# Optimization experiments

Measured on AMD Instinct MI355X. Metric: run time of the kernel, lower is better.

Reference implementation:

```python
import jax, jax.numpy as jnp
import numpy as np

DIM = 4096
N_HEADS = 32
N_KV_HEADS = 8
HEAD_DIM = DIM // N_HEADS      # 128
N_REP = N_HEADS // N_KV_HEADS  # 4
B, S = 2, 2048
THETA = 10000.0


def _rope_tables(seq_len, head_dim):
    # standard llama2.c freqs: [1, S, 1, head_dim//2]
    freqs = 1.0 / (THETA ** (np.arange(0, head_dim, 2, dtype=np.float32) / head_dim))
    t = np.arange(seq_len, dtype=np.float32)
    ang = np.outer(t, freqs)  # [S, head_dim//2]
    cos = jnp.asarray(np.cos(ang))[None, :, None, :]
    sin = jnp.asarray(np.sin(ang))[None, :, None, :]
    return cos, sin


def setup_inputs() -> dict:
    key = jax.random.key(0)
    ks = jax.random.split(key, 5)
    x = jax.random.normal(ks[0], (B, S, DIM), dtype=jnp.float32)
    freqs_cos, freqs_sin = _rope_tables(S, HEAD_DIM)
    scale = 1.0 / np.sqrt(DIM)
    wq = jax.random.normal(ks[1], (DIM, N_HEADS * HEAD_DIM), dtype=jnp.float32) * scale
    wk = jax.random.normal(ks[2], (DIM, N_KV_HEADS * HEAD_DIM), dtype=jnp.float32) * scale
    wv = jax.random.normal(ks[3], (DIM, N_KV_HEADS * HEAD_DIM), dtype=jnp.float32) * scale
    wo = jax.random.normal(ks[4], (N_HEADS * HEAD_DIM, DIM), dtype=jnp.float32) * scale
    return {"x": x, "freqs_cos": freqs_cos, "freqs_sin": freqs_sin,
            "wq": wq, "wk": wk, "wv": wv, "wo": wo}


def _apply_rotary(t, cos, sin):
    # t: [B, S, H, head_dim]; cos/sin: [1, S, 1, head_dim//2]
    b, s, h, d = t.shape
    tr = t.reshape(b, s, h, d // 2, 2)
    t_r, t_i = tr[..., 0], tr[..., 1]
    out_r = t_r * cos - t_i * sin
    out_i = t_r * sin + t_i * cos
    return jnp.stack([out_r, out_i], axis=-1).reshape(b, s, h, d)


def reference(x, freqs_cos, freqs_sin, wq, wk, wv, wo):
    b, s, _ = x.shape
    q = (x @ wq).reshape(b, s, N_HEADS, HEAD_DIM)
    k = (x @ wk).reshape(b, s, N_KV_HEADS, HEAD_DIM)
    v = (x @ wv).reshape(b, s, N_KV_HEADS, HEAD_DIM)
    q = _apply_rotary(q, freqs_cos, freqs_sin)
    k = _apply_rotary(k, freqs_cos, freqs_sin)
    # GQA: repeat kv heads to match q heads
    k = jnp.repeat(k, N_REP, axis=2)  # [b, s, H, hd]
    v = jnp.repeat(v, N_REP, axis=2)
    # NOTE: source calls SDPA with attn_mask=None and no is_causal -> non-causal
    scores = jnp.einsum('bqhd,bkhd->bhqk', q, k) / jnp.sqrt(
        jnp.asarray(HEAD_DIM, dtype=q.dtype))
    attn = jax.nn.softmax(scores, axis=-1)
    out = jnp.einsum('bhqk,bkhd->bqhd', attn, v)
    out = out.reshape(b, s, N_HEADS * HEAD_DIM)
    return out @ wo
```

## Files before the change

### kernel.cpp

```cpp
#include <hip/hip_runtime.h>
#include <cstdint>


typedef __attribute__((ext_vector_type(8))) short short8;
typedef __attribute__((ext_vector_type(4))) float f32x4;
typedef __attribute__((ext_vector_type(16))) float f32x16;

__device__ __forceinline__ float bf2f(unsigned short u) {
  union { unsigned int i; float f; } v; v.i = ((unsigned int)u) << 16; return v.f;
}
__device__ __forceinline__ unsigned short f2bf(float f) {
  union { float f; unsigned int i; } v; v.f = f;
  unsigned int r = v.i + 0x7fffu + ((v.i >> 16) & 1u);
  return (unsigned short)(r >> 16);
}

__device__ __forceinline__ void gload_lds16(const void* g, void* lds) {
  __builtin_amdgcn_global_load_lds(
      (const __attribute__((address_space(1))) unsigned int*)g,
      (__attribute__((address_space(3))) unsigned int*)lds, 16, 0, 0);
}

__device__ __forceinline__ unsigned int cvtpk_bf16(float lo, float hi) {
  unsigned int r;
  asm("v_cvt_pk_bf16_f32 %0, %1, %2" : "=v"(r) : "v"(lo), "v"(hi));
  return r;
}
__device__ __forceinline__ void pl32swap(unsigned int& a, unsigned int& b) {
  asm("v_permlane32_swap_b32 %0, %1" : "+v"(a), "+v"(b));
}


__global__ __launch_bounds__(256) void prepass(const float* __restrict__ x,
                                               const float* __restrict__ wq,
                                               const float* __restrict__ wk,
                                               const float* __restrict__ wv,
                                               const float* __restrict__ wo,
                                               unsigned short* __restrict__ xbf,
                                               unsigned short* __restrict__ wqkvT,
                                               unsigned short* __restrict__ woT) {
  __shared__ float tile[32][33];
  const int b = blockIdx.x;
  if (b < 16384) {
    size_t i = (size_t)b * 256 + threadIdx.x;
    float4 v = ((const float4*)x)[i];
    ushort4 o; o.x = f2bf(v.x); o.y = f2bf(v.y); o.z = f2bf(v.z); o.w = f2bf(v.w);
    ((ushort4*)xbf)[i] = o;
    return;
  }
  int tx = threadIdx.x & 31, ty = threadIdx.x >> 5;
  const float* src; int c0, C, gc0, r0;
  unsigned short* dst; int ldd;
  if (b < 16384 + 24576) {
    int t = b - 16384;
    gc0 = (t % 192) * 32; r0 = (t / 192) * 32;
    if (gc0 < 4096)      { src = wq; c0 = gc0;        C = 4096; }
    else if (gc0 < 5120) { src = wk; c0 = gc0 - 4096; C = 1024; }
    else                 { src = wv; c0 = gc0 - 5120; C = 1024; }
    dst = wqkvT; ldd = 4096;
  } else {
    int t = b - 40960;
    gc0 = (t % 128) * 32; r0 = (t / 128) * 32;
    src = wo; c0 = gc0; C = 4096;
    dst = woT; ldd = 4096;
  }
#pragma unroll
  for (int j = 0; j < 4; ++j)
    tile[ty + j * 8][tx] = src[(size_t)(r0 + ty + j * 8) * C + c0 + tx];
  __syncthreads();
#pragma unroll
  for (int j = 0; j < 4; ++j)
    dst[(size_t)(gc0 + ty + j * 8) * ldd + r0 + tx] = f2bf(tile[tx][ty + j * 8]);
}

__global__ __launch_bounds__(256) void rope_kk(unsigned short* __restrict__ qkv,
                                               const float* __restrict__ cosT,
                                               const float* __restrict__ sinT) {
  int idx = blockIdx.x * 256 + threadIdx.x;
  int t = idx >> 7;
  int cb = (idx & 127) * 8;
  int s = t & 2047;
  int j0 = (cb & 127) >> 1;
  unsigned short* p = qkv + (size_t)t * 6144 + 4096 + cb;
  uint4 u = *(const uint4*)p;
  float4 c4 = *(const float4*)&cosT[s * 64 + j0];
  float4 s4 = *(const float4*)&sinT[s * 64 + j0];
  auto rot = [](unsigned int& uu, float c, float sn) {
    float re = bf2f((unsigned short)(uu & 0xffffu));
    float im = bf2f((unsigned short)(uu >> 16));
    float nr = re * c - im * sn;
    float ni = re * sn + im * c;
    uu = (unsigned int)f2bf(nr) | ((unsigned int)f2bf(ni) << 16);
  };
  rot(u.x, c4.x, s4.x); rot(u.y, c4.y, s4.y);
  rot(u.z, c4.z, s4.z); rot(u.w, c4.w, s4.w);
  *(uint4*)p = u;
}


#define GBAR() asm volatile("s_barrier" ::: "memory")
#define GVM6() asm volatile("s_waitcnt vmcnt(6)" ::: "memory")
#define GVM4() asm volatile("s_waitcnt vmcnt(4)" ::: "memory")
#define GHINT() asm volatile("s_waitcnt lgkmcnt(8)" ::: "memory")

#define GLDA(buf, mh)                                                                   \
  do {                                                                                  \
    _Pragma("unroll") for (int m_ = 0; m_ < 4; ++m_)                                    \
    _Pragma("unroll") for (int ks_ = 0; ks_ < 2; ++ks_)                                 \
      a[m_][ks_] = *(const short8*)&smem[buf][0]                                        \
          [(wm * 128 + (mh) * 64 + m_ * 16 + lr) * 64 + (((ks_ * 4 + lg) ^ (lr & 7)) << 3)]; \
  } while (0)

#define GLDB(bf_, buf, nh)                                                              \
  do {                                                                                  \
    _Pragma("unroll") for (int n_ = 0; n_ < 2; ++n_)                                    \
    _Pragma("unroll") for (int ks_ = 0; ks_ < 2; ++ks_)                                 \
      bf_[n_][ks_] = *(const short8*)&smem[buf][1]                                      \
          [(wn * 64 + (nh) * 32 + n_ * 16 + lr) * 64 + (((ks_ * 4 + lg) ^ (lr & 7)) << 3)]; \
  } while (0)

#define GMM(bf_, mh, nh)                                                                \
  do {                                                                                  \
    __builtin_amdgcn_s_setprio(1);                                                      \
    _Pragma("unroll") for (int ks_ = 0; ks_ < 2; ++ks_)                                 \
    _Pragma("unroll") for (int m_ = 0; m_ < 4; ++m_)                                    \
    _Pragma("unroll") for (int n_ = 0; n_ < 2; ++n_)                                    \
      acc[(mh) * 4 + m_][(nh) * 2 + n_] = __builtin_amdgcn_mfma_f32_16x16x32_bf16(      \
          a[m_][ks_], bf_[n_][ks_], acc[(mh) * 4 + m_][(nh) * 2 + n_], 0, 0, 0);        \
    __builtin_amdgcn_s_setprio(0);                                                      \
  } while (0)

#define GSTG(half, buf, tile)                                                           \
  do {                                                                                  \
    _Pragma("unroll") for (int t2_ = 0; t2_ < 2; ++t2_)                                 \
      gload_lds16(srcp[half][t2_] + ((size_t)(tile) << 6),                              \
                  &smem[buf][(half) >> 1][dsto[half][t2_]]);                            \
  } while (0)

template <typename OutT>
__device__ __forceinline__ void gemm256_body(const unsigned short* __restrict__ A,
                                             const unsigned short* __restrict__ B,
                                             OutT* __restrict__ C, int K, int ldc,
                                             int bid,
                                             unsigned short (*smem)[2][16384]) {
  const int xcd = bid & 7, ii = bid >> 3;
  const int mt = (xcd & 3) * 4 + (ii & 3);
  const int nt = (xcd >> 2) * 8 + (ii >> 2);
  const int m0 = mt * 256, n0 = nt * 256;
  const int tid = threadIdx.x, w = tid >> 6, l = tid & 63;
  const int wm = w >> 2, wn = w & 3;
  const int lr = l & 15, lg = l >> 4;
  const int NT = K >> 6;

  const int lsub = l >> 3, lgr = l & 7;
  const int sg = (lgr ^ lsub) << 3;
  const unsigned short* srcp[4][2];
  int dsto[4][2];
#pragma unroll
  for (int t2 = 0; t2 < 2; ++t2) {
    int lb = t2 * 64 + w * 8;
    int pa0 = (lb & 63) + ((lb >> 6) << 7);
    int pb0 = (lb & 31) + ((lb >> 5) << 6);
    srcp[0][t2] = A + (size_t)(m0 + pa0 + lsub) * K + sg;       dsto[0][t2] = pa0 * 64;
    srcp[1][t2] = A + (size_t)(m0 + pa0 + 64 + lsub) * K + sg;  dsto[1][t2] = (pa0 + 64) * 64;
    srcp[2][t2] = B + (size_t)(n0 + pb0 + lsub) * K + sg;       dsto[2][t2] = pb0 * 64;
    srcp[3][t2] = B + (size_t)(n0 + pb0 + 32 + lsub) * K + sg;  dsto[3][t2] = (pb0 + 32) * 64;
  }

  f32x4 acc[8][4] = {};
  short8 a[4][2], b0f[2][2], b1f[2][2];

  GSTG(0, 0, 0); GSTG(2, 0, 0); GSTG(3, 0, 0); GSTG(1, 0, 0);
  GSTG(0, 1, 1); GSTG(2, 1, 1); GSTG(3, 1, 1);
  GVM6();
  GBAR();

  for (int t = 0; t < NT / 2; ++t) {
    const int t1 = 2 * t + 1;
    const int t2a = (2 * t + 2 < NT) ? 2 * t + 2 : NT - 1;
    const int t2b = (2 * t + 3 < NT) ? 2 * t + 3 : NT - 1;
    GLDA(0, 0); GLDB(b0f, 0, 0);
    GSTG(1, 1, t1);
    GHINT();
    GBAR(); GMM(b0f, 0, 0); GBAR();
    GLDB(b1f, 0, 1);
    GSTG(0, 0, t2a);
    GBAR(); GMM(b1f, 0, 1); GBAR();
    GLDA(0, 1);
    GSTG(2, 0, t2a);
    GBAR(); GMM(b0f, 1, 0); GBAR();
    GSTG(3, 0, t2a);
    GBAR(); GMM(b1f, 1, 1); GVM6(); GBAR();
    GLDA(1, 0); GLDB(b0f, 1, 0);
    GSTG(1, 0, t2a);
    GHINT();
    GBAR(); GMM(b0f, 0, 0); GBAR();
    GLDB(b1f, 1, 1);
    GSTG(0, 1, t2b);
    GBAR(); GMM(b1f, 0, 1); GBAR();
    GLDA(1, 1);
    GSTG(2, 1, t2b);
    GBAR(); GMM(b0f, 1, 0); GBAR();
    GSTG(3, 1, t2b);
    GBAR(); GMM(b1f, 1, 1); GVM6(); GBAR();
  }

#pragma unroll
  for (int m = 0; m < 8; ++m)
#pragma unroll
    for (int n = 0; n < 4; ++n)
#pragma unroll
      for (int r = 0; r < 4; ++r) {
        int row = m0 + wm * 128 + m * 16 + lg * 4 + r;
        int col = n0 + wn * 64 + n * 16 + lr;
        float v = acc[m][n][r];
        if constexpr (sizeof(OutT) == 2)
          C[(size_t)row * ldc + col] = (OutT)f2bf(v);
        else
          C[(size_t)row * ldc + col] = v;
      }
}


#define KLDA(buf)                                                                       \
  do {                                                                                  \
    _Pragma("unroll") for (int m_ = 0; m_ < 4; ++m_)                                    \
    _Pragma("unroll") for (int ks_ = 0; ks_ < 2; ++ks_)                                 \
      a2[m_][ks_] = *(const short8*)&As2[buf]                                           \
          [(wm * 64 + m_ * 16 + lr) * 64 + (((ks_ * 4 + lg) ^ (lr & 7)) << 3)];         \
  } while (0)

#define KLDB(bf_, buf, nh)                                                              \
  do {                                                                                  \
    _Pragma("unroll") for (int n_ = 0; n_ < 2; ++n_)                                    \
    _Pragma("unroll") for (int ks_ = 0; ks_ < 2; ++ks_)                                 \
      bf_[n_][ks_] = *(const short8*)&Bs2[buf]                                          \
          [(wn * 64 + (nh) * 32 + n_ * 16 + lr) * 64 + (((ks_ * 4 + lg) ^ (lr & 7)) << 3)]; \
  } while (0)

#define KMM(bf_, nh)                                                                    \
  do {                                                                                  \
    __builtin_amdgcn_s_setprio(1);                                                      \
    _Pragma("unroll") for (int ks_ = 0; ks_ < 2; ++ks_)                                 \
    _Pragma("unroll") for (int m_ = 0; m_ < 4; ++m_)                                    \
    _Pragma("unroll") for (int n_ = 0; n_ < 2; ++n_)                                    \
      acc[m_][(nh) * 2 + n_] = __builtin_amdgcn_mfma_f32_16x16x32_bf16(                 \
          a2[m_][ks_], bf_[n_][ks_], acc[m_][(nh) * 2 + n_], 0, 0, 0);                  \
    __builtin_amdgcn_s_setprio(0);                                                      \
  } while (0)

#define KSTGA(buf, tile)                                                                \
  do {                                                                                  \
    _Pragma("unroll") for (int t2_ = 0; t2_ < 2; ++t2_)                                 \
      gload_lds16(srcA[t2_] + ((size_t)(tile) << 6), &As2[buf][dstA[t2_]]);             \
  } while (0)
#define KSTGB0(buf, tile)                                                               \
  do {                                                                                  \
    _Pragma("unroll") for (int t2_ = 0; t2_ < 2; ++t2_)                                 \
      gload_lds16(srcB0[t2_] + ((size_t)(tile) << 6), &Bs2[buf][dstB0[t2_]]);           \
  } while (0)
#define KSTGB1(buf, tile)                                                               \
  do {                                                                                  \
    _Pragma("unroll") for (int t2_ = 0; t2_ < 2; ++t2_)                                 \
      gload_lds16(srcB1[t2_] + ((size_t)(tile) << 6), &Bs2[buf][dstB1[t2_]]);           \
  } while (0)

__device__ __forceinline__ void kvproj_body(const unsigned short* __restrict__ A,
                                            const unsigned short* __restrict__ B,
                                            unsigned short* __restrict__ C,
                                            unsigned short* __restrict__ vt,
                                            int K, int ldc, int bid,
                                            unsigned short (*As2)[8192],
                                            unsigned short (*Bs2)[16384]) {
  const int xcd = bid & 7, ii = bid >> 3;
  const int mt = (xcd & 3) * 8 + (ii & 7);
  const int nt = (xcd >> 2) * 4 + (ii >> 3);
  const int m0 = mt * 128, n0 = nt * 256;
  const int tid = threadIdx.x, w = tid >> 6, l = tid & 63;
  const int wm = w >> 2, wn = w & 3;
  const int lr = l & 15, lg = l >> 4;
  const int NT = K >> 6;

  const int lsub = l >> 3, lgr = l & 7;
  const int sg = (lgr ^ lsub) << 3;
  const unsigned short* srcA[2];  int dstA[2];
  const unsigned short* srcB0[2]; int dstB0[2];
  const unsigned short* srcB1[2]; int dstB1[2];
#pragma unroll
  for (int t2 = 0; t2 < 2; ++t2) {
    int ra = t2 * 64 + w * 8;
    srcA[t2] = A + (size_t)(m0 + ra + lsub) * K + sg;            dstA[t2] = ra * 64;
    int lb = t2 * 64 + w * 8;
    int pb0 = (lb & 31) + ((lb >> 5) << 6);
    srcB0[t2] = B + (size_t)(n0 + pb0 + lsub) * K + sg;          dstB0[t2] = pb0 * 64;
    srcB1[t2] = B + (size_t)(n0 + pb0 + 32 + lsub) * K + sg;     dstB1[t2] = (pb0 + 32) * 64;
  }

  f32x4 acc[4][4] = {};
  short8 a2[4][2], bb0[2][2], bb1[2][2];

  KSTGA(0, 0); KSTGB0(0, 0); KSTGB1(0, 0);
  KSTGA(1, 1); KSTGB0(1, 1);
  GVM4();
  GBAR();

  for (int t = 0; t < NT / 2; ++t) {
    const int t1 = 2 * t + 1;
    const int t2a = (2 * t + 2 < NT) ? 2 * t + 2 : NT - 1;
    const int t2b = (2 * t + 3 < NT) ? 2 * t + 3 : NT - 1;
    KLDA(0); KLDB(bb0, 0, 0);
    KSTGB1(1, t1);
    GHINT();
    GBAR(); KMM(bb0, 0); GBAR();
    KLDB(bb1, 0, 1);
    KSTGA(0, t2a); KSTGB0(0, t2a);
    GBAR(); KMM(bb1, 1); GVM4(); GBAR();
    KLDA(1); KLDB(bb0, 1, 0);
    KSTGB1(0, t2a);
    GHINT();
    GBAR(); KMM(bb0, 0); GBAR();
    KLDB(bb1, 1, 1);
    KSTGA(1, t2b); KSTGB0(1, t2b);
    GBAR(); KMM(bb1, 1); GVM4(); GBAR();
  }

  if (n0 >= 1024) {
#pragma unroll
    for (int m = 0; m < 4; ++m)
#pragma unroll
      for (int n = 0; n < 4; ++n) {
        const int col = n0 + wn * 64 + n * 16 + lr;
        const int kvh = (col - 1024) >> 7, d = (col - 1024) & 127;
        const int row0 = m0 + wm * 64 + m * 16 + lg * 4;
        const int bb = row0 >> 11, tok = row0 & 2047;
        ushort4 o;
        o.x = f2bf(acc[m][n][0]); o.y = f2bf(acc[m][n][1]);
        o.z = f2bf(acc[m][n][2]); o.w = f2bf(acc[m][n][3]);
        *(ushort4*)&vt[(size_t)((bb * 8 + kvh) * 128 + d) * 2048 + tok] = o;
      }
  } else {
#pragma unroll
    for (int m = 0; m < 4; ++m)
#pragma unroll
      for (int n = 0; n < 4; ++n)
#pragma unroll
        for (int r = 0; r < 4; ++r) {
          int row = m0 + wm * 64 + m * 16 + lg * 4 + r;
          int col = n0 + wn * 64 + n * 16 + lr;
          C[(size_t)row * ldc + col] = f2bf(acc[m][n][r]);
        }
  }
}

__global__ __launch_bounds__(512) void gemm_qkv(const unsigned short* __restrict__ A,
                                                const unsigned short* __restrict__ Bq,
                                                const unsigned short* __restrict__ Bkv,
                                                unsigned short* __restrict__ qkv,
                                                unsigned short* __restrict__ vt) {
  __shared__ unsigned short smem[2][2][16384];
  const int bid = blockIdx.x;
  if (bid < 256) {
    gemm256_body<unsigned short>(A, Bq, qkv, 4096, 6144, bid, smem);
  } else {
    unsigned short (*As2)[8192]  = (unsigned short (*)[8192])&smem[0][0][0];
    unsigned short (*Bs2)[16384] = (unsigned short (*)[16384])(&smem[0][0][0] + 16384);
    kvproj_body(A, Bkv, qkv + 4096, vt, 4096, 6144, bid - 256, As2, Bs2);
  }
}

__global__ __launch_bounds__(512) void gemm_oproj(const unsigned short* __restrict__ A,
                                                  const unsigned short* __restrict__ B,
                                                  float* __restrict__ C,
                                                  int K, int ldc) {
  __shared__ unsigned short smem[2][2][16384];
  gemm256_body<float>(A, B, C, K, ldc, blockIdx.x, smem);
}


__global__ __launch_bounds__(256, 2) void attn_k(const unsigned short* __restrict__ qkv,
                                                 const unsigned short* __restrict__ vt,
                                                 const float* __restrict__ fc,
                                                 const float* __restrict__ fs,
                                                 unsigned short* __restrict__ ctx) {
  __shared__ unsigned short Ks[2][64 * 128];
  __shared__ unsigned short Vs[3][128 * 64];
  const int bid = blockIdx.x;
  const int xcd = bid & 7, idx = bid >> 3;
  const int kvg = xcd * 2 + (idx >> 6);
  const int hg = (idx >> 4) & 3;
  const int qt = idx & 15;
  const int b = kvg >> 3, kvh = kvg & 7, h = kvh * 4 + hg;
  const int w = threadIdx.x >> 6, l = threadIdx.x & 63;
  const int lc = l & 31, hi = l >> 5;
  const size_t tok0 = (size_t)b * 2048;
  const int q0 = qt * 128 + w * 32;
  const float C2 = 0.12751744516557944f;

  const unsigned short* ksrc[4];
  const unsigned short* vsrc[4];
#pragma unroll
  for (int i = 0; i < 4; ++i) {
    int L = w * 256 + i * 64 + l;
    int krow = L >> 4, kc = L & 15;
    ksrc[i] = qkv + (tok0 + krow) * 6144 + 4096 + kvh * 128 + ((kc ^ (krow & 7)) << 3);
    int vrow = L >> 3, vc = L & 7;
    vsrc[i] = vt + (size_t)(kvg * 128 + vrow) * 2048 + ((vc ^ (vrow & 7)) << 3);
  }
  const int ldsBase = (w * 256) * 8;

  auto stageK = [&](int bufi, int kv0s) {
#pragma unroll
    for (int i = 0; i < 4; ++i)
      gload_lds16(ksrc[i] + (size_t)kv0s * 6144, &Ks[bufi][ldsBase + i * 512]);
  };
  auto stageV = [&](int bufi, int kv0s) {
#pragma unroll
    for (int i = 0; i < 4; ++i)
      gload_lds16(vsrc[i] + kv0s, &Vs[bufi][ldsBase + i * 512]);
  };

  const unsigned short* Qb = qkv + (tok0 + q0 + lc) * 6144 + h * 128 + hi * 8;
  const int s = q0 + lc;
  short8 qf[8];
#pragma unroll
  for (int dc = 0; dc < 8; ++dc) {
    uint4 raw = *(const uint4*)(Qb + dc * 16);
    float4 c4 = *(const float4*)&fc[s * 64 + dc * 8 + hi * 4];
    float4 s4 = *(const float4*)&fs[s * 64 + dc * 8 + hi * 4];
    auto rotw = [C2](unsigned int uu, float c, float sn) -> unsigned int {
      float re = bf2f((unsigned short)(uu & 0xffffu));
      float im = bf2f((unsigned short)(uu >> 16));
      return cvtpk_bf16((re * c - im * sn) * C2, (re * sn + im * c) * C2);
    };
    union { unsigned int u[4]; short8 v; } t;
    t.u[0] = rotw(raw.x, c4.x, s4.x);
    t.u[1] = rotw(raw.y, c4.y, s4.y);
    t.u[2] = rotw(raw.z, c4.z, s4.z);
    t.u[3] = rotw(raw.w, c4.w, s4.w);
    qf[dc] = t.v;
  }

  f32x16 acc[4] = {};
  float lsum = 0.f;

  stageK(0, 0);
  stageV(0, 0);
  stageV(1, 64);
  __syncthreads();

  int kb = 0, vb = 0;
  const int swz = (lc & 7) << 3;
  for (int kt = 0; kt < 32; ++kt) {
    const int nk = (kt + 1 < 32) ? kt + 1 : 31;
    const int nv = (kt + 2 < 32) ? kt + 2 : 31;
    int vs2 = vb + 2; if (vs2 >= 3) vs2 -= 3;
    stageK(kb ^ 1, nk * 64);
    stageV(vs2, nv * 64);
    f32x16 s0 = {}, s1 = {};
    __builtin_amdgcn_s_setprio(1);
#pragma unroll
    for (int dc = 0; dc < 8; ++dc) {
      int cidx = ((dc * 2 + hi) << 3) ^ swz;
      short8 kf0 = *(const short8*)&Ks[kb][lc * 128 + cidx];
      short8 kf1 = *(const short8*)&Ks[kb][(lc + 32) * 128 + cidx];
      s0 = __builtin_amdgcn_mfma_f32_32x32x16_bf16(kf0, qf[dc], s0, 0, 0, 0);
      s1 = __builtin_amdgcn_mfma_f32_32x32x16_bf16(kf1, qf[dc], s1, 0, 0, 0);
    }
    __builtin_amdgcn_s_setprio(0);
    float p[32];
    short8 pa[4];
#pragma unroll
    for (int g = 0; g < 4; ++g) {
#pragma unroll
      for (int j = 0; j < 8; ++j) {
        float sv = (g < 2) ? s0[g * 8 + j] : s1[(g - 2) * 8 + j];
        p[g * 8 + j] = __builtin_amdgcn_exp2f(sv);
      }
      unsigned int c0 = cvtpk_bf16(p[g * 8 + 0], p[g * 8 + 1]);
      unsigned int c1 = cvtpk_bf16(p[g * 8 + 2], p[g * 8 + 3]);
      unsigned int c2 = cvtpk_bf16(p[g * 8 + 4], p[g * 8 + 5]);
      unsigned int c3 = cvtpk_bf16(p[g * 8 + 6], p[g * 8 + 7]);
      pl32swap(c0, c2);
      pl32swap(c1, c3);
      union { unsigned int u[4]; short8 v; } t;
      t.u[0] = c0; t.u[1] = c1; t.u[2] = c2; t.u[3] = c3;
      pa[g] = t.v;
    }
    __builtin_amdgcn_s_setprio(1);
#pragma unroll
    for (int ks = 0; ks < 4; ++ks) {
#pragma unroll
      for (int dt = 0; dt < 4; ++dt) {
        short8 vf = *(const short8*)&Vs[vb][(dt * 32 + lc) * 64 + ((((ks * 2 + hi) << 3) ^ swz))];
        acc[dt] = __builtin_amdgcn_mfma_f32_32x32x16_bf16(pa[ks], vf, acc[dt], 0, 0, 0);
      }
    }
    __builtin_amdgcn_s_setprio(0);
#pragma unroll
    for (int r = 0; r < 32; ++r) lsum += p[r];
    asm volatile("s_waitcnt vmcnt(4)" ::: "memory");
    asm volatile("s_barrier" ::: "memory");
    kb ^= 1;
    vb = (vb + 1 == 3) ? 0 : vb + 1;
  }
  lsum += __shfl_xor(lsum, 32, 64);
  float rl = 1.0f / lsum;
#pragma unroll
  for (int r = 0; r < 16; ++r) {
    int crow = (r & 3) + 8 * (r >> 2) + 4 * hi;
    float rlr = __shfl(rl, crow, 64);
    unsigned short* cp = ctx + (tok0 + q0 + crow) * 4096 + h * 128 + lc;
#pragma unroll
    for (int dt = 0; dt < 4; ++dt) cp[dt * 32] = f2bf(acc[dt][r] * rlr);
  }
}


extern "C" void kernel_launch(void* const* d_in, const int* in_sizes, int n_in,
                              void* d_out, int out_size, void* d_ws, size_t ws_size,
                              hipStream_t stream) {
  const float* x  = (const float*)d_in[0];
  const float* fc = (const float*)d_in[1];
  const float* fs = (const float*)d_in[2];
  const float* wq = (const float*)d_in[3];
  const float* wk = (const float*)d_in[4];
  const float* wv = (const float*)d_in[5];
  const float* wo = (const float*)d_in[6];
  float* out = (float*)d_out;
  char* ws = (char*)d_ws;

  constexpr size_t SZ_WQKVT = (size_t)6144 * 4096 * 2;
  constexpr size_t SZ_WOT   = (size_t)4096 * 4096 * 2;
  constexpr size_t SZ_QKV   = (size_t)4096 * 6144 * 2;
  constexpr size_t SZ_VT    = (size_t)16 * 128 * 2048 * 2;

  unsigned short* wqkvT = (unsigned short*)ws;
  unsigned short* woT   = (unsigned short*)(ws + SZ_WQKVT);
  unsigned short* qkv   = (unsigned short*)(ws + SZ_WQKVT + SZ_WOT);
  unsigned short* vt    = (unsigned short*)(ws + SZ_WQKVT + SZ_WOT + SZ_QKV);
  unsigned short* xbf   = (unsigned short*)(ws + SZ_WQKVT + SZ_WOT + SZ_QKV + SZ_VT);
  unsigned short* ctx   = xbf;

  prepass<<<57344, 256, 0, stream>>>(x, wq, wk, wv, wo, xbf, wqkvT, woT);
  gemm_qkv<<<512, 512, 0, stream>>>(xbf, wqkvT, wqkvT + (size_t)4096 * 4096, qkv, vt);
  rope_kk<<<2048, 256, 0, stream>>>(qkv, fc, fs);
  attn_k<<<1024, 256, 0, stream>>>(qkv, vt, fc, fs, ctx);
  gemm_oproj<<<256, 512, 0, stream>>>(ctx, woT, out, 4096, 4096);
}
```

Baseline: 496.4 us.

## Split-K the KV projection into uniform 256x256 tiles with a reduce kernel

The KV projection blocks in the QKV GEMM launch now reuse the 256x256 gemm body with split-K=2, so all 512 blocks run the same tile shape and get balanced work. The two bf16 partial sums are written to a workspace, and a new reduce kernel adds them, applies RoPE to K and transposes V into the vt layout. This replaces the separate kvproj path and rope kernel when the workspace is large enough. In exchange it adds extra global traffic for the partials, an extra rounding of the partials to bf16, and a transpose kernel.

Measured after the change: 496.4 us. No clear change (+0.0%).

```diff
diff --git a/kernel.cpp b/kernel.cpp
--- a/kernel.cpp
+++ b/kernel.cpp
@@ -97,6 +97,57 @@
   *(uint4*)p = u;
 }
 
+__global__ __launch_bounds__(256) void reduce_kv(const unsigned short* __restrict__ p0,
+                                                 const unsigned short* __restrict__ p1,
+                                                 unsigned short* __restrict__ qkv,
+                                                 unsigned short* __restrict__ vt,
+                                                 const float* __restrict__ cosT,
+                                                 const float* __restrict__ sinT) {
+  __shared__ float tile[32][33];
+  const int b = blockIdx.x;
+  if (b < 2048) {
+    int idx = b * 256 + threadIdx.x;
+    int t = idx >> 7;
+    int cb = (idx & 127) * 8;
+    int s = t & 2047;
+    int j0 = (cb & 127) >> 1;
+    const size_t off = (size_t)t * 2048 + cb;
+    uint4 u0 = *(const uint4*)(p0 + off);
+    uint4 u1 = *(const uint4*)(p1 + off);
+    float4 c4 = *(const float4*)&cosT[s * 64 + j0];
+    float4 s4 = *(const float4*)&sinT[s * 64 + j0];
+    auto comb = [](unsigned int a, unsigned int bb, float c, float sn) -> unsigned int {
+      float re = bf2f((unsigned short)(a & 0xffffu)) + bf2f((unsigned short)(bb & 0xffffu));
+      float im = bf2f((unsigned short)(a >> 16)) + bf2f((unsigned short)(bb >> 16));
+      float nr = re * c - im * sn;
+      float ni = re * sn + im * c;
+      return (unsigned int)f2bf(nr) | ((unsigned int)f2bf(ni) << 16);
+    };
+    uint4 o;
+    o.x = comb(u0.x, u1.x, c4.x, s4.x);
+    o.y = comb(u0.y, u1.y, c4.y, s4.y);
+    o.z = comb(u0.z, u1.z, c4.z, s4.z);
+    o.w = comb(u0.w, u1.w, c4.w, s4.w);
+    *(uint4*)(qkv + (size_t)t * 6144 + 4096 + cb) = o;
+    return;
+  }
+  const int t = b - 2048;
+  const int tok0t = (t & 63) * 32;
+  const int d0 = ((t >> 6) & 3) * 32;
+  const int bk = t >> 8;
+  const int bb = bk >> 3, kvh = bk & 7;
+  const int tx = threadIdx.x & 31, ty = threadIdx.x >> 5;
+#pragma unroll
+  for (int j = 0; j < 4; ++j) {
+    size_t off = (size_t)(bb * 2048 + tok0t + ty + j * 8) * 2048 + 1024 + kvh * 128 + d0 + tx;
+    tile[ty + j * 8][tx] = bf2f(p0[off]) + bf2f(p1[off]);
+  }
+  __syncthreads();
+#pragma unroll
+  for (int j = 0; j < 4; ++j)
+    vt[(size_t)(bk * 128 + d0 + ty + j * 8) * 2048 + tok0t + tx] = f2bf(tile[tx][ty + j * 8]);
+}
+
 
 #define GBAR() asm volatile("s_barrier" ::: "memory")
 #define GVM6() asm volatile("s_waitcnt vmcnt(6)" ::: "memory")
@@ -140,17 +191,13 @@
 template <typename OutT>
 __device__ __forceinline__ void gemm256_body(const unsigned short* __restrict__ A,
                                              const unsigned short* __restrict__ B,
-                                             OutT* __restrict__ C, int K, int ldc,
-                                             int bid,
+                                             OutT* __restrict__ C, int Kext, int lda,
+                                             int ldc, int m0, int n0,
                                              unsigned short (*smem)[2][16384]) {
-  const int xcd = bid & 7, ii = bid >> 3;
-  const int mt = (xcd & 3) * 4 + (ii & 3);
-  const int nt = (xcd >> 2) * 8 + (ii >> 2);
-  const int m0 = mt * 256, n0 = nt * 256;
   const int tid = threadIdx.x, w = tid >> 6, l = tid & 63;
   const int wm = w >> 2, wn = w & 3;
   const int lr = l & 15, lg = l >> 4;
-  const int NT = K >> 6;
+  const int NT = Kext >> 6;
 
   const int lsub = l >> 3, lgr = l & 7;
   const int sg = (lgr ^ lsub) << 3;
@@ -161,10 +208,10 @@
     int lb = t2 * 64 + w * 8;
     int pa0 = (lb & 63) + ((lb >> 6) << 7);
     int pb0 = (lb & 31) + ((lb >> 5) << 6);
-    srcp[0][t2] = A + (size_t)(m0 + pa0 + lsub) * K + sg;       dsto[0][t2] = pa0 * 64;
-    srcp[1][t2] = A + (size_t)(m0 + pa0 + 64 + lsub) * K + sg;  dsto[1][t2] = (pa0 + 64) * 64;
-    srcp[2][t2] = B + (size_t)(n0 + pb0 + lsub) * K + sg;       dsto[2][t2] = pb0 * 64;
-    srcp[3][t2] = B + (size_t)(n0 + pb0 + 32 + lsub) * K + sg;  dsto[3][t2] = (pb0 + 32) * 64;
+    srcp[0][t2] = A + (size_t)(m0 + pa0 + lsub) * lda + sg;       dsto[0][t2] = pa0 * 64;
+    srcp[1][t2] = A + (size_t)(m0 + pa0 + 64 + lsub) * lda + sg;  dsto[1][t2] = (pa0 + 64) * 64;
+    srcp[2][t2] = B + (size_t)(n0 + pb0 + lsub) * lda + sg;       dsto[2][t2] = pb0 * 64;
+    srcp[3][t2] = B + (size_t)(n0 + pb0 + 32 + lsub) * lda + sg;  dsto[3][t2] = (pb0 + 32) * 64;
   }
 
   f32x4 acc[8][4] = {};
@@ -352,19 +399,46 @@
   }
 }
 
-__global__ __launch_bounds__(512) void gemm_qkv(const unsigned short* __restrict__ A,
-                                                const unsigned short* __restrict__ Bq,
-                                                const unsigned short* __restrict__ Bkv,
-                                                unsigned short* __restrict__ qkv,
-                                                unsigned short* __restrict__ vt) {
+__global__ __launch_bounds__(512) void gemm_qkv_fb(const unsigned short* __restrict__ A,
+                                                   const unsigned short* __restrict__ Bq,
+                                                   const unsigned short* __restrict__ Bkv,
+                                                   unsigned short* __restrict__ qkv,
+                                                   unsigned short* __restrict__ vt) {
   __shared__ unsigned short smem[2][2][16384];
   const int bid = blockIdx.x;
   if (bid < 256) {
-    gemm256_body<unsigned short>(A, Bq, qkv, 4096, 6144, bid, smem);
+    const int xcd = bid & 7, ii = bid >> 3;
+    const int mt = (xcd & 3) * 4 + (ii & 3);
+    const int nt = (xcd >> 2) * 8 + (ii >> 2);
+    gemm256_body<unsigned short>(A, Bq, qkv, 4096, 4096, 6144, mt * 256, nt * 256, smem);
   } else {
     unsigned short (*As2)[8192]  = (unsigned short (*)[8192])&smem[0][0][0];
     unsigned short (*Bs2)[16384] = (unsigned short (*)[16384])(&smem[0][0][0] + 16384);
     kvproj_body(A, Bkv, qkv + 4096, vt, 4096, 6144, bid - 256, As2, Bs2);
+  }
+}
+
+__global__ __launch_bounds__(512) void gemm_qkv_sp(const unsigned short* __restrict__ A,
+                                                   const unsigned short* __restrict__ Bq,
+                                                   const unsigned short* __restrict__ Bkv,
+                                                   unsigned short* __restrict__ qkv,
+                                                   unsigned short* __restrict__ pws) {
+  __shared__ unsigned short smem[2][2][16384];
+  const int bid = blockIdx.x;
+  if (bid < 256) {
+    const int xcd = bid & 7, ii = bid >> 3;
+    const int mt = (xcd & 3) * 4 + (ii & 3);
+    const int nt = (xcd >> 2) * 8 + (ii >> 2);
+    gemm256_body<unsigned short>(A, Bq, qkv, 4096, 4096, 6144, mt * 256, nt * 256, smem);
+  } else {
+    const int b2 = (bid - 256) & 127;
+    const int sp = (bid - 256) >> 7;
+    const int xcd = b2 & 7, ii = b2 >> 3;
+    const int mt = (xcd & 3) * 4 + (ii & 3);
+    const int nt = (xcd >> 2) * 4 + (ii >> 2);
+    gemm256_body<unsigned short>(A + sp * 2048, Bkv + sp * 2048,
+                                 pws + (size_t)sp * 4096 * 2048,
+                                 2048, 4096, 2048, mt * 256, nt * 256, smem);
   }
 }
 
@@ -373,7 +447,11 @@
                                                   float* __restrict__ C,
                                                   int K, int ldc) {
   __shared__ unsigned short smem[2][2][16384];
-  gemm256_body<float>(A, B, C, K, ldc, blockIdx.x, smem);
+  const int bid = blockIdx.x;
+  const int xcd = bid & 7, ii = bid >> 3;
+  const int mt = (xcd & 3) * 4 + (ii & 3);
+  const int nt = (xcd >> 2) * 8 + (ii >> 2);
+  gemm256_body<float>(A, B, C, K, K, ldc, mt * 256, nt * 256, smem);
 }
 
 
@@ -533,6 +611,9 @@
   constexpr size_t SZ_WOT   = (size_t)4096 * 4096 * 2;
   constexpr size_t SZ_QKV   = (size_t)4096 * 6144 * 2;
   constexpr size_t SZ_VT    = (size_t)16 * 128 * 2048 * 2;
+  constexpr size_t SZ_XBF   = (size_t)4096 * 4096 * 2;
+  constexpr size_t SZ_BASE  = SZ_WQKVT + SZ_WOT + SZ_QKV + SZ_VT + SZ_XBF;
+  constexpr size_t SZ_PWS   = (size_t)2 * 4096 * 2048 * 2;
 
   unsigned short* wqkvT = (unsigned short*)ws;
   unsigned short* woT   = (unsigned short*)(ws + SZ_WQKVT);
@@ -540,10 +621,18 @@
   unsigned short* vt    = (unsigned short*)(ws + SZ_WQKVT + SZ_WOT + SZ_QKV);
   unsigned short* xbf   = (unsigned short*)(ws + SZ_WQKVT + SZ_WOT + SZ_QKV + SZ_VT);
   unsigned short* ctx   = xbf;
+  unsigned short* pws   = (unsigned short*)(ws + SZ_BASE);
+
+  const bool useSplit = (ws_size >= SZ_BASE + SZ_PWS);
 
   prepass<<<57344, 256, 0, stream>>>(x, wq, wk, wv, wo, xbf, wqkvT, woT);
-  gemm_qkv<<<512, 512, 0, stream>>>(xbf, wqkvT, wqkvT + (size_t)4096 * 4096, qkv, vt);
-  rope_kk<<<2048, 256, 0, stream>>>(qkv, fc, fs);
+  if (useSplit) {
+    gemm_qkv_sp<<<512, 512, 0, stream>>>(xbf, wqkvT, wqkvT + (size_t)4096 * 4096, qkv, pws);
+    reduce_kv<<<6144, 256, 0, stream>>>(pws, pws + (size_t)4096 * 2048, qkv, vt, fc, fs);
+  } else {
+    gemm_qkv_fb<<<512, 512, 0, stream>>>(xbf, wqkvT, wqkvT + (size_t)4096 * 4096, qkv, vt);
+    rope_kk<<<2048, 256, 0, stream>>>(qkv, fc, fs);
+  }
   attn_k<<<1024, 256, 0, stream>>>(qkv, vt, fc, fs, ctx);
   gemm_oproj<<<256, 512, 0, stream>>>(ctx, woT, out, 4096, 4096);
 }
```
